# Kernel tuning notes

Measured on AMD Instinct MI355X. Metric: run time of the kernel, lower is better.

## Reference

```python
import jax, jax.numpy as jnp
import numpy as np

B = 16384        # batch_size
T_BINS = 128     # t_bins
Z_BINS = 128     # z_bins
Z_LO, Z_HI = -1.0, 1.0
Z_STD, T_STD = 0.1, 0.1
EPS = 0.01


def setup_inputs() -> dict:
    key = jax.random.key(0)
    k1, k2, k3 = jax.random.split(key, 3)
    z = jax.random.normal(k1, (B, 1), dtype=jnp.float32)
    t = jax.random.uniform(k2, (B, 1), dtype=jnp.float32)
    # buffers built exactly as in __init__
    t_means = jnp.linspace(0.0, 1.0, T_BINS, dtype=jnp.float32)
    z_edges = jnp.linspace(Z_LO, Z_HI, Z_BINS + 1, dtype=jnp.float32)
    z_means = 0.5 * (z_edges[1:] + z_edges[:-1])
    zz, tt = jnp.meshgrid(z_means, t_means, indexing='ij')  # torch default 'ij'
    means = jnp.stack([zz, tt], axis=-1)                     # (Z_BINS, T_BINS, 2)
    # weights buffer starts at zero in the module; use small positive values
    weights = jax.random.uniform(k3, (Z_BINS, T_BINS, 1), dtype=jnp.float32) * 0.1
    return {"z": z, "t": t, "means": means, "weights": weights}


def reference(z, t, means, weights):
    # log_density: z (B,1), t (B,1) -> (B,1)
    zt = jnp.concatenate([z, t], axis=1)              # (B, 2)
    m = means.reshape(-1, 2)                          # (M, 2), M = Z_BINS*T_BINS
    inv_var = jnp.array([1.0 / Z_STD**2, 1.0 / T_STD**2], dtype=zt.dtype)
    # pairwise squared distances scaled per-dim: (B, M)
    diff = jnp.square(zt[:, None, :] - m[None, :, :])  # (B, M, 2)
    unweighted_potential = -0.5 * jnp.sum(diff * inv_var, axis=-1)
    weighted_potential = unweighted_potential + jnp.log(weights.reshape(1, -1) + EPS)
    return -jnp.sum(jnp.exp(weighted_potential), axis=1, keepdims=True)  # (B, 1)
```

## Files before the change

kernel.cpp:

```cpp
#include <hip/hip_runtime.h>


namespace {

constexpr float C2   = 72.13475204444817f;
constexpr float EPSW = 0.01f;

typedef __attribute__((ext_vector_type(8))) short bf16x8;
typedef __attribute__((ext_vector_type(4))) float f32x4;

__device__ inline unsigned short bf16rn(float x) {
    unsigned u = __builtin_bit_cast(unsigned, x);
    return (unsigned short)((u + 0x7fffu + ((u >> 16) & 1u)) >> 16);
}

__global__ __launch_bounds__(256) void gkb_density_kernel(
    const float* __restrict__ z,
    const float* __restrict__ t,
    const float* __restrict__ w,
    float* __restrict__ out)
{
    __shared__ unsigned short Wb[128 * 128];
    __shared__ float zs[64], ts[64];

    const int tid = threadIdx.x;
    const int b0  = blockIdx.x * 64;

    if (tid < 64)        zs[tid]      = z[b0 + tid];
    else if (tid < 128)  ts[tid - 64] = t[b0 + tid - 64];

    {
        const int i  = tid >> 1;
        const int c0 = (tid & 1) * 64;
        const float* __restrict__ src = w + i * 128 + c0;
        unsigned short* dst = &Wb[i * 128 + c0];
#pragma unroll
        for (int c = 0; c < 64; c += 4) {
            float4 v = *(const float4*)(src + c);
            dst[c + 0] = bf16rn(v.x + EPSW);
            dst[c + 1] = bf16rn(v.y + EPSW);
            dst[c + 2] = bf16rn(v.z + EPSW);
            dst[c + 3] = bf16rn(v.w + EPSW);
        }
    }
    __syncthreads();

    const int lane = tid & 63;
    const int wv   = tid >> 6;
    const int m    = lane & 15;
    const int quad = lane >> 4;
    const int bw   = b0 + wv * 16;

    const float tb = ts[wv * 16 + m];
    bf16x8 Af[4];
#pragma unroll
    for (int kt = 0; kt < 4; ++kt) {
#pragma unroll
        for (int jj = 0; jj < 8; ++jj) {
            const int k  = kt * 32 + quad * 8 + jj;
            const float dt = tb - (float)k * (1.0f / 127.0f);
            const float v  = __builtin_amdgcn_exp2f(-C2 * dt * dt);
            Af[kt][jj] = (short)bf16rn(v);
        }
    }

    float zr[4];
#pragma unroll
    for (int r = 0; r < 4; ++r) zr[r] = zs[wv * 16 + quad * 4 + r];

    float S[4] = {0.f, 0.f, 0.f, 0.f};
#pragma unroll
    for (int it = 0; it < 8; ++it) {
        f32x4 acc = {0.f, 0.f, 0.f, 0.f};
#pragma unroll
        for (int kt = 0; kt < 4; ++kt) {
            const bf16x8 Bf = *(const bf16x8*)&Wb[(it * 16 + m) * 128 + kt * 32 + quad * 8];
            acc = __builtin_amdgcn_mfma_f32_16x16x32_bf16(Af[kt], Bf, acc, 0, 0, 0);
        }
        const int   i  = it * 16 + m;
        const float zm = -1.0f + (float)(2 * i + 1) * 0.0078125f;
#pragma unroll
        for (int r = 0; r < 4; ++r) {
            const float dz = zr[r] - zm;
            const float E  = __builtin_amdgcn_exp2f(-C2 * dz * dz);
            S[r] = fmaf(E, acc[r], S[r]);
        }
    }

#pragma unroll
    for (int d = 1; d < 16; d <<= 1) {
#pragma unroll
        for (int r = 0; r < 4; ++r) S[r] += __shfl_xor(S[r], d, 64);
    }
    if (m == 0) {
#pragma unroll
        for (int r = 0; r < 4; ++r) out[bw + quad * 4 + r] = -S[r];
    }
}

}

extern "C" void kernel_launch(void* const* d_in, const int* in_sizes, int n_in,
                              void* d_out, int out_size, void* d_ws, size_t ws_size,
                              hipStream_t stream) {
    const float* z = (const float*)d_in[0];
    const float* t = (const float*)d_in[1];
    const float* w = (const float*)d_in[3];
    float* out = (float*)d_out;

    const int B = in_sizes[0];
    dim3 block(256);
    dim3 grid(B / 64);
    gkb_density_kernel<<<grid, block, 0, stream>>>(z, t, w, out);
}
```

Before: 62.87 us.

## Pad LDS weight tile, coalesce weight loads, overlap staging with A-fragment math

Restructures the weight staging so each thread issues 16 coalesced float4 loads across rows, computes the Gaussian A fragments while those loads are in flight, then writes packed 4-wide bf16 values into an LDS tile padded to a row stride of 136. The z/t shared staging is dropped in favor of direct global reads. The padding is meant to remove LDS bank conflicts on the MFMA B-fragment reads and on the packed stores. The early issue is meant to hide global latency behind the exp2 work. The cost is higher register pressure from holding 16 float4 values, which could reduce occupancy.

```diff
diff --git a/kernel.cpp b/kernel.cpp
--- a/kernel.cpp
+++ b/kernel.cpp
@@ -5,9 +5,11 @@
 
 constexpr float C2   = 72.13475204444817f;
 constexpr float EPSW = 0.01f;
+constexpr int   LDW  = 136;
 
 typedef __attribute__((ext_vector_type(8))) short bf16x8;
 typedef __attribute__((ext_vector_type(4))) float f32x4;
+typedef __attribute__((ext_vector_type(4))) unsigned short u16x4;
 
 __device__ inline unsigned short bf16rn(float x) {
     unsigned u = __builtin_bit_cast(unsigned, x);
@@ -20,38 +22,24 @@
     const float* __restrict__ w,
     float* __restrict__ out)
 {
-    __shared__ unsigned short Wb[128 * 128];
-    __shared__ float zs[64], ts[64];
+    __shared__ unsigned short Wb[128 * LDW];
 
-    const int tid = threadIdx.x;
-    const int b0  = blockIdx.x * 64;
-
-    if (tid < 64)        zs[tid]      = z[b0 + tid];
-    else if (tid < 128)  ts[tid - 64] = t[b0 + tid - 64];
-
-    {
-        const int i  = tid >> 1;
-        const int c0 = (tid & 1) * 64;
-        const float* __restrict__ src = w + i * 128 + c0;
-        unsigned short* dst = &Wb[i * 128 + c0];
-#pragma unroll
-        for (int c = 0; c < 64; c += 4) {
-            float4 v = *(const float4*)(src + c);
-            dst[c + 0] = bf16rn(v.x + EPSW);
-            dst[c + 1] = bf16rn(v.y + EPSW);
-            dst[c + 2] = bf16rn(v.z + EPSW);
-            dst[c + 3] = bf16rn(v.w + EPSW);
-        }
-    }
-    __syncthreads();
-
+    const int tid  = threadIdx.x;
+    const int b0   = blockIdx.x * 64;
     const int lane = tid & 63;
     const int wv   = tid >> 6;
     const int m    = lane & 15;
     const int quad = lane >> 4;
     const int bw   = b0 + wv * 16;
 
-    const float tb = ts[wv * 16 + m];
+    const int jj0 = 4 * (tid & 31);
+    const int i0  = tid >> 5;
+    float4 v[16];
+#pragma unroll
+    for (int c = 0; c < 16; ++c)
+        v[c] = *(const float4*)(w + (i0 + 8 * c) * 128 + jj0);
+
+    const float tb = t[bw + m];
     bf16x8 Af[4];
 #pragma unroll
     for (int kt = 0; kt < 4; ++kt) {
@@ -59,14 +47,23 @@
         for (int jj = 0; jj < 8; ++jj) {
             const int k  = kt * 32 + quad * 8 + jj;
             const float dt = tb - (float)k * (1.0f / 127.0f);
-            const float v  = __builtin_amdgcn_exp2f(-C2 * dt * dt);
-            Af[kt][jj] = (short)bf16rn(v);
+            Af[kt][jj] = (short)bf16rn(__builtin_amdgcn_exp2f(-C2 * dt * dt));
         }
     }
-
     float zr[4];
 #pragma unroll
-    for (int r = 0; r < 4; ++r) zr[r] = zs[wv * 16 + quad * 4 + r];
+    for (int r = 0; r < 4; ++r) zr[r] = z[bw + quad * 4 + r];
+
+#pragma unroll
+    for (int c = 0; c < 16; ++c) {
+        u16x4 p;
+        p[0] = bf16rn(v[c].x + EPSW);
+        p[1] = bf16rn(v[c].y + EPSW);
+        p[2] = bf16rn(v[c].z + EPSW);
+        p[3] = bf16rn(v[c].w + EPSW);
+        *(u16x4*)&Wb[(i0 + 8 * c) * LDW + jj0] = p;
+    }
+    __syncthreads();
 
     float S[4] = {0.f, 0.f, 0.f, 0.f};
 #pragma unroll
@@ -74,7 +71,7 @@
         f32x4 acc = {0.f, 0.f, 0.f, 0.f};
 #pragma unroll
         for (int kt = 0; kt < 4; ++kt) {
-            const bf16x8 Bf = *(const bf16x8*)&Wb[(it * 16 + m) * 128 + kt * 32 + quad * 8];
+            const bf16x8 Bf = *(const bf16x8*)&Wb[(it * 16 + m) * LDW + kt * 32 + quad * 8];
             acc = __builtin_amdgcn_mfma_f32_16x16x32_bf16(Af[kt], Bf, acc, 0, 0, 0);
         }
         const int   i  = it * 16 + m;
```

Result: faster. 60.76 us (-3.4%).
